# Kernel tuning notes

Measured on AMD Instinct MI355X. Metric: run time of the kernel, lower is better.

## Reference

```python
import jax, jax.numpy as jnp
import numpy as np

H = 1024
F = 4096  # base_ffn_dim = hidden * 4
WIDTHS = [256, 512]  # adapters; idx 2 -> width==hidden -> identity
EPS = 1e-5


def _xavier(key, fan_in, fan_out, gain):
    a = gain * np.sqrt(6.0 / (fan_in + fan_out))
    return jax.random.uniform(key, (fan_in, fan_out), jnp.float32, -a, a)


def _layernorm(x, g, b):
    mu = jnp.mean(x, axis=-1, keepdims=True)
    var = jnp.var(x, axis=-1, keepdims=True)
    return (x - mu) * jax.lax.rsqrt(var + EPS) * g + b


def setup_inputs() -> dict:
    key = jax.random.key(0)
    ks = jax.random.split(key, 12)
    g = 1.0 / np.sqrt(2.0)
    B, S = 4, 2048
    return {
        "x": jax.random.normal(ks[0], (B, S, H), jnp.float32),
        "width_multiplier": jax.random.uniform(ks[1], (B, S, 1), jnp.float32),
        "width_idx": jax.random.randint(ks[2], (B, S), 0, 3, jnp.int32),
        "ln_in_g": jnp.ones((H,), jnp.float32),
        "ln_in_b": jnp.zeros((H,), jnp.float32),
        "W1": _xavier(ks[3], H, F, g),
        "b1": jnp.zeros((F,), jnp.float32),
        "ln_h_g": jnp.ones((F,), jnp.float32),
        "ln_h_b": jnp.zeros((F,), jnp.float32),
        "W2": _xavier(ks[4], F, H, g),
        "b2": jnp.zeros((H,), jnp.float32),
        "a256_w1": _xavier(ks[5], H, 256, g),
        "a256_b1": jnp.zeros((256,), jnp.float32),
        "a256_w2": _xavier(ks[6], 256, H, g),
        "a256_b2": jnp.zeros((H,), jnp.float32),
        "a512_w1": _xavier(ks[7], H, 512, g),
        "a512_b1": jnp.zeros((512,), jnp.float32),
        "a512_w2": _xavier(ks[8], 512, H, g),
        "a512_b2": jnp.zeros((H,), jnp.float32),
    }


def reference(x, width_multiplier, width_idx,
              ln_in_g, ln_in_b, W1, b1, ln_h_g, ln_h_b, W2, b2,
              a256_w1, a256_b1, a256_w2, a256_b2,
              a512_w1, a512_b1, a512_w2, a512_b2):
    gelu = lambda t: jax.nn.gelu(t, approximate=False)  # torch nn.GELU exact
    x_norm = _layernorm(x, ln_in_g, ln_in_b)
    # base FFN path
    h = gelu(jnp.einsum("bsh,hf->bsf", x_norm, W1) + b1)
    h = _layernorm(h, ln_h_g, ln_h_b)
    base = jnp.einsum("bsf,fh->bsh", h, W2) + b2
    # width adapters (routed per token by width_idx)
    ad0 = jnp.einsum("bsw,wh->bsh", gelu(jnp.einsum("bsh,hw->bsw", x_norm, a256_w1) + a256_b1), a256_w2) + a256_b2
    ad1 = jnp.einsum("bsw,wh->bsh", gelu(jnp.einsum("bsh,hw->bsw", x_norm, a512_w1) + a512_b1), a512_w2) + a512_b2
    idx = width_idx[..., None]
    adaptive = jnp.where(idx == 0, ad0, jnp.where(idx == 1, ad1, x_norm))
    return base * width_multiplier + adaptive * (1.0 - width_multiplier)
```

## Files before the change

### kernel.cpp

```cpp
#include <hip/hip_runtime.h>
#include <cstdint>
#include <cstddef>

typedef unsigned short u16x8 __attribute__((ext_vector_type(8)));
typedef unsigned short u16x4 __attribute__((ext_vector_type(4)));
typedef __bf16 bf16x8 __attribute__((ext_vector_type(8)));
typedef float f32x4 __attribute__((ext_vector_type(4)));

__device__ __forceinline__ float b2f(unsigned short u) {
    union { unsigned int i; float f; } v;
    v.i = ((unsigned int)u) << 16;
    return v.f;
}

__device__ __forceinline__ unsigned short f2b(float f) {
    union { float f; unsigned int i; } v;
    v.f = f;
    unsigned int x = v.i;
    unsigned int lsb = (x >> 16) & 1u;
    x += 0x7FFFu + lsb;
    return (unsigned short)(x >> 16);
}

__device__ __forceinline__ float gelu_exact(float x) {
    return 0.5f * x * (1.0f + erff(x * 0.70710678118654752f));
}

__device__ __forceinline__ void ld_lds16(const unsigned short* g, unsigned short* l) {
    __builtin_amdgcn_global_load_lds(
        (const __attribute__((address_space(1))) void*)g,
        (__attribute__((address_space(3))) void*)l, 16, 0, 0);
}

__global__ void transpose_f32_bf16(const float* __restrict__ in,
                                   unsigned short* __restrict__ out, int R, int C,
                                   const float* __restrict__ scale) {
    __shared__ float tile[32][33];
    int x = blockIdx.x * 32 + threadIdx.x;
    int y0 = blockIdx.y * 32;
    for (int k = 0; k < 32; k += 8)
        tile[threadIdx.y + k][threadIdx.x] = in[(size_t)(y0 + threadIdx.y + k) * C + x];
    __syncthreads();
    int ox = y0 + threadIdx.x;
    int oy = blockIdx.x * 32;
    float sc = scale ? scale[ox] : 1.0f;
    for (int k = 0; k < 32; k += 8)
        out[(size_t)(oy + threadIdx.y + k) * R + ox] = f2b(tile[threadIdx.x][threadIdx.y + k] * sc);
}

__global__ void concat_bias(const float* __restrict__ b0, const float* __restrict__ b1,
                            float* __restrict__ out) {
    int t = threadIdx.x + blockIdx.x * blockDim.x;
    if (t < 256) out[t] = b0[t];
    else if (t < 768) out[t] = b1[t - 256];
}

__global__ void init_c01(const float* __restrict__ b2, float* __restrict__ c0b2,
                         float* __restrict__ c1) {
    int n = blockIdx.x * 256 + threadIdx.x;
    c0b2[n] = b2[n];
    c1[n] = 0.0f;
}

__global__ void prep_c01(const float* __restrict__ W2, const float* __restrict__ g,
                         const float* __restrict__ b, float* __restrict__ c0b2,
                         float* __restrict__ c1, int K, int N) {
    int n = blockIdx.x * 256 + threadIdx.x;
    int k0 = blockIdx.y * 256;
    float p0 = 0.f, p1 = 0.f;
    for (int k = k0; k < k0 + 256; ++k) {
        float w = W2[(size_t)k * N + n];
        p0 += b[k] * w;
        p1 += g[k] * w;
    }
    atomicAdd(&c0b2[n], p0);
    atomicAdd(&c1[n], p1);
}

__global__ __launch_bounds__(256) void rowstats4096(const unsigned short* __restrict__ h,
                                                    float* __restrict__ st) {
    const int row = blockIdx.x;
    const int t = threadIdx.x;
    const u16x8* p = (const u16x8*)(h + (size_t)row * 4096);
    float s = 0.f, s2 = 0.f;
#pragma unroll
    for (int i = 0; i < 2; ++i) {
        u16x8 v = p[t + (i << 8)];
#pragma unroll
        for (int r = 0; r < 8; ++r) { float f = b2f(v[r]); s += f; s2 += f * f; }
    }
#pragma unroll
    for (int o = 32; o > 0; o >>= 1) {
        s  += __shfl_down(s, o, 64);
        s2 += __shfl_down(s2, o, 64);
    }
    __shared__ float red[8];
    int lane = t & 63, w = t >> 6;
    if (lane == 0) { red[w] = s; red[4 + w] = s2; }
    __syncthreads();
    if (t == 0) {
        float ss = red[0] + red[1] + red[2] + red[3];
        float qq = red[4] + red[5] + red[6] + red[7];
        const float inv = 1.0f / 4096.0f;
        float mu = ss * inv;
        float var = qq * inv - mu * mu;
        float rs = rsqrtf(var + 1e-5f);
        st[2 * (size_t)row]     = rs;
        st[2 * (size_t)row + 1] = rs * mu;
    }
}

__global__ __launch_bounds__(256) void ln1024(const float* __restrict__ in,
                                              unsigned short* __restrict__ out,
                                              const float* __restrict__ g,
                                              const float* __restrict__ b) {
    const int row = blockIdx.x;
    const int t = threadIdx.x;
    f32x4 v = ((const f32x4*)(in + (size_t)row * 1024))[t];
    float s = v[0] + v[1] + v[2] + v[3];
    float s2 = v[0] * v[0] + v[1] * v[1] + v[2] * v[2] + v[3] * v[3];
#pragma unroll
    for (int o = 32; o > 0; o >>= 1) {
        s  += __shfl_down(s, o, 64);
        s2 += __shfl_down(s2, o, 64);
    }
    __shared__ float red[8];
    int lane = t & 63, w = t >> 6;
    if (lane == 0) { red[w] = s; red[4 + w] = s2; }
    __syncthreads();
    if (t == 0) {
        red[0] = red[0] + red[1] + red[2] + red[3];
        red[4] = red[4] + red[5] + red[6] + red[7];
    }
    __syncthreads();
    const float inv_n = 1.0f / 1024.0f;
    float mu = red[0] * inv_n;
    float var = red[4] * inv_n - mu * mu;
    float rs = rsqrtf(var + 1e-5f);
    f32x4 gv = ((const f32x4*)g)[t];
    f32x4 bv = ((const f32x4*)b)[t];
    u16x4 ov;
#pragma unroll
    for (int r = 0; r < 4; ++r) ov[r] = f2b((v[r] - mu) * rs * gv[r] + bv[r]);
    ((u16x4*)(out + (size_t)row * 1024))[t] = ov;
}

__global__ __launch_bounds__(512, 2) void gemm256_gelu(
    const unsigned short* __restrict__ A, int lda,
    const unsigned short* __restrict__ BT, int ldb,
    const float* __restrict__ bias, unsigned short* __restrict__ Cb,
    int M, int N, int K) {
    __shared__ __align__(16) unsigned short As[2][256 * 64];
    __shared__ __align__(16) unsigned short Bs[2][256 * 64];

    const int t = threadIdx.x;

    int id = blockIdx.y * gridDim.x + blockIdx.x;
    const int nwg = gridDim.x * gridDim.y;
    {
        const int cpx = nwg >> 3;
        id = (id & 7) * cpx + (id >> 3);
    }
    const int m0 = (id / gridDim.x) * 256;
    const int n0 = (id % gridDim.x) * 256;

    const int lane = t & 63;
    const int wid = t >> 6;
    const int wmr = (wid >> 2) << 7;
    const int wnr = (wid & 3) << 6;
    const int ml = lane & 15;
    const int q = lane >> 4;

    const int srow8 = lane >> 3;
    const int scol = (((lane & 7) ^ (srow8 & 7)) << 3);

    const int c0 = ((q ^ (ml & 7)) << 3);
    const int c1 = c0 ^ 32;

    f32x4 acc[8][4];
#pragma unroll
    for (int i = 0; i < 8; ++i)
#pragma unroll
        for (int j = 0; j < 4; ++j)
#pragma unroll
            for (int r = 0; r < 4; ++r) acc[i][j][r] = 0.0f;

    const int nk = K >> 6;

#define STAGE256(KT, BUF)                                                       \
    {                                                                           \
        const unsigned short* asrc =                                            \
            A + (size_t)(m0 + wid * 8 + srow8) * lda + (KT) * 64 + scol;        \
        const unsigned short* bsrc =                                            \
            BT + (size_t)(n0 + wid * 8 + srow8) * ldb + (KT) * 64 + scol;       \
        _Pragma("unroll")                                                       \
        for (int s = 0; s < 4; ++s) {                                           \
            ld_lds16(asrc + (size_t)s * 64 * lda, &As[BUF][(s * 64 + wid * 8) * 64]); \
            ld_lds16(bsrc + (size_t)s * 64 * ldb, &Bs[BUF][(s * 64 + wid * 8) * 64]); \
        }                                                                       \
    }

#define LDA256(QI)                                                              \
    _Pragma("unroll")                                                           \
    for (int i2 = 0; i2 < 4; ++i2) {                                            \
        int row = wmr + (QI) * 64 + i2 * 16 + ml;                               \
        afq[i2][0] = *(const bf16x8*)(&As[cur][(row << 6) + c0]);               \
        afq[i2][1] = *(const bf16x8*)(&As[cur][(row << 6) + c1]);               \
    }

#define LDB256(DST, QJ)                                                         \
    _Pragma("unroll")                                                           \
    for (int j2 = 0; j2 < 2; ++j2) {                                            \
        int row = wnr + (QJ) * 32 + j2 * 16 + ml;                               \
        DST[j2][0] = *(const bf16x8*)(&Bs[cur][(row << 6) + c0]);               \
        DST[j2][1] = *(const bf16x8*)(&Bs[cur][(row << 6) + c1]);               \
    }

#define MFMA16(I0, J0, BF)                                                      \
    __builtin_amdgcn_s_barrier();                                               \
    __builtin_amdgcn_s_setprio(1);                                              \
    _Pragma("unroll")                                                           \
    for (int i2 = 0; i2 < 4; ++i2)                                              \
        _Pragma("unroll")                                                       \
        for (int j2 = 0; j2 < 2; ++j2) {                                        \
            acc[(I0) + i2][(J0) + j2] = __builtin_amdgcn_mfma_f32_16x16x32_bf16( \
                afq[i2][0], BF[j2][0], acc[(I0) + i2][(J0) + j2], 0, 0, 0);     \
            acc[(I0) + i2][(J0) + j2] = __builtin_amdgcn_mfma_f32_16x16x32_bf16( \
                afq[i2][1], BF[j2][1], acc[(I0) + i2][(J0) + j2], 0, 0, 0);     \
        }                                                                       \
    __builtin_amdgcn_s_setprio(0);                                              \
    __builtin_amdgcn_s_barrier();

    STAGE256(0, 0);
    for (int kt = 0; kt < nk; ++kt) {
        const int cur = kt & 1;
        if (kt + 1 < nk) {
            STAGE256(kt + 1, cur ^ 1);
            asm volatile("s_waitcnt vmcnt(8)" ::: "memory");
        } else {
            asm volatile("s_waitcnt vmcnt(0)" ::: "memory");
        }
        __builtin_amdgcn_s_barrier();

        bf16x8 afq[4][2], b0f[2][2], b1f[2][2];
        LDA256(0);
        LDB256(b0f, 0);
        MFMA16(0, 0, b0f);
        LDB256(b1f, 1);
        MFMA16(0, 2, b1f);
        LDA256(1);
        MFMA16(4, 2, b1f);
        MFMA16(4, 0, b0f);
    }
#undef STAGE256
#undef LDA256
#undef LDB256
#undef MFMA16

#pragma unroll
    for (int i = 0; i < 8; ++i) {
#pragma unroll
        for (int j = 0; j < 4; ++j) {
            int col = n0 + wnr + j * 16 + ml;
            float bv = bias[col];
#pragma unroll
            for (int r = 0; r < 4; ++r) {
                int row = m0 + wmr + i * 16 + q * 4 + r;
                Cb[(size_t)row * N + col] = f2b(gelu_exact(acc[i][j][r] + bv));
            }
        }
    }
}

template <int EPI>
__global__ __launch_bounds__(256) void gemm_bt(
    const unsigned short* __restrict__ A, int lda,
    const unsigned short* __restrict__ BT, int ldb,
    const float* __restrict__ bias, unsigned short* __restrict__ Cb,
    float* __restrict__ Cf, int M, int N, int K,
    const int* __restrict__ idx, int match,
    const float* __restrict__ wm,
    const unsigned short* __restrict__ adaptive,
    const unsigned short* __restrict__ xn,
    const float* __restrict__ c1v,
    const float* __restrict__ rstat) {
    __shared__ __align__(16) unsigned short As[2][128 * 32];
    __shared__ __align__(16) unsigned short Bs[2][128 * 32];

    const int t = threadIdx.x;

    int id = blockIdx.y * gridDim.x + blockIdx.x;
    const int nwg = gridDim.x * gridDim.y;
    if ((nwg & 7) == 0) {
        const int cpx = nwg >> 3;
        id = (id & 7) * cpx + (id >> 3);
    }
    const int bx = id % gridDim.x;
    const int by = id / gridDim.x;
    const int m0 = by * 128;
    const int n0 = bx * 128;

    const int lane = t & 63;
    const int wid = t >> 6;

    const int srow = lane >> 2;
    const int sch  = (lane & 3) ^ (srow & 3);
    const int scol = sch << 3;

    const int wr = (wid >> 1) << 6;
    const int wc = (wid & 1) << 6;
    const int ml = lane & 15;
    const int q = lane >> 4;
    const int qsw = ((q ^ (ml & 3)) << 3);

    f32x4 acc[4][4];
#pragma unroll
    for (int i = 0; i < 4; ++i)
#pragma unroll
        for (int j = 0; j < 4; ++j)
#pragma unroll
            for (int r = 0; r < 4; ++r) acc[i][j][r] = 0.0f;

    const int nk = K >> 5;

#define STAGE(KT, BUF)                                                          \
    {                                                                           \
        _Pragma("unroll")                                                       \
        for (int hh = 0; hh < 2; ++hh) {                                        \
            int rbase = wid * 32 + hh * 16;                                     \
            int row = rbase + srow;                                             \
            ld_lds16(A  + (size_t)(m0 + row) * lda + (KT) * 32 + scol,          \
                     &As[BUF][rbase * 32]);                                     \
            ld_lds16(BT + (size_t)(n0 + row) * ldb + (KT) * 32 + scol,          \
                     &Bs[BUF][rbase * 32]);                                     \
        }                                                                       \
    }

    STAGE(0, 0);
    for (int kt = 0; kt < nk; ++kt) {
        const int cur = kt & 1;
        __syncthreads();
        if (kt + 1 < nk) STAGE(kt + 1, cur ^ 1);

        bf16x8 af[4], bf[4];
#pragma unroll
        for (int i = 0; i < 4; ++i)
            af[i] = *(const bf16x8*)(&As[cur][(wr + i * 16 + ml) * 32 + qsw]);
#pragma unroll
        for (int j = 0; j < 4; ++j)
            bf[j] = *(const bf16x8*)(&Bs[cur][(wc + j * 16 + ml) * 32 + qsw]);
#pragma unroll
        for (int i = 0; i < 4; ++i)
#pragma unroll
            for (int j = 0; j < 4; ++j)
                acc[i][j] = __builtin_amdgcn_mfma_f32_16x16x32_bf16(af[i], bf[j], acc[i][j], 0, 0, 0);
    }
#undef STAGE

#pragma unroll
    for (int i = 0; i < 4; ++i) {
        float rsv[4], rmv[4], wv[4];
        int idv[4];
        if (EPI == 1 || EPI == 2) {
#pragma unroll
            for (int r = 0; r < 4; ++r) {
                int row = m0 + wr + i * 16 + q * 4 + r;
                idv[r] = idx[row];
                if (EPI == 2) {
                    wv[r] = wm[row];
                    rsv[r] = rstat[2 * (size_t)row];
                    rmv[r] = rstat[2 * (size_t)row + 1];
                }
            }
        }
#pragma unroll
        for (int j = 0; j < 4; ++j) {
            int col = n0 + wc + j * 16 + ml;
            float bv = bias[col];
            float c1c = (EPI == 2) ? c1v[col] : 0.0f;
#pragma unroll
            for (int r = 0; r < 4; ++r) {
                int row = m0 + wr + i * 16 + q * 4 + r;
                size_t off = (size_t)row * N + col;
                if (EPI == 0) {
                    Cb[off] = f2b(gelu_exact(acc[i][j][r] + bv));
                } else if (EPI == 1) {
                    if (idv[r] == match) Cb[off] = f2b(acc[i][j][r] + bv);
                } else {
                    float bval = rsv[r] * acc[i][j][r] + bv - rmv[r] * c1c;
                    float a = b2f((idv[r] <= 1) ? adaptive[off] : xn[off]);
                    Cf[off] = bval * wv[r] + a * (1.0f - wv[r]);
                }
            }
        }
    }
}

extern "C" void kernel_launch(void* const* d_in, const int* in_sizes, int n_in,
                              void* d_out, int out_size, void* d_ws, size_t ws_size,
                              hipStream_t stream) {
    const float* x       = (const float*)d_in[0];
    const float* wm      = (const float*)d_in[1];
    const int*   widx    = (const int*)d_in[2];
    const float* ln_in_g = (const float*)d_in[3];
    const float* ln_in_b = (const float*)d_in[4];
    const float* W1      = (const float*)d_in[5];
    const float* b1      = (const float*)d_in[6];
    const float* ln_h_g  = (const float*)d_in[7];
    const float* ln_h_b  = (const float*)d_in[8];
    const float* W2      = (const float*)d_in[9];
    const float* b2      = (const float*)d_in[10];
    const float* a256_w1 = (const float*)d_in[11];
    const float* a256_b1 = (const float*)d_in[12];
    const float* a256_w2 = (const float*)d_in[13];
    const float* a256_b2 = (const float*)d_in[14];
    const float* a512_w1 = (const float*)d_in[15];
    const float* a512_b1 = (const float*)d_in[16];
    const float* a512_w2 = (const float*)d_in[17];
    const float* a512_b2 = (const float*)d_in[18];
    float* out = (float*)d_out;

    const int T = 8192, H = 1024, F = 4096;

    unsigned short* ws0   = (unsigned short*)d_ws;
    unsigned short* xn    = ws0;
    unsigned short* h     = xn    + (size_t)T * H;
    unsigned short* tt    = h     + (size_t)T * F;
    unsigned short* adp   = tt    + (size_t)T * 768;
    unsigned short* W1T   = adp   + (size_t)T * H;
    unsigned short* W2T   = W1T   + (size_t)H * F;
    unsigned short* awup  = W2T   + (size_t)F * H;
    unsigned short* aw2T0 = awup  + (size_t)768 * H;
    unsigned short* aw2T1 = aw2T0 + (size_t)H * 256;
    float*          ab1   = (float*)(aw2T1 + (size_t)H * 512);
    float*          stats = ab1 + 768;
    float*          c0b2  = stats + (size_t)T * 2;
    float*          c1    = c0b2 + H;

    dim3 tb(32, 8);
    init_c01<<<H / 256, 256, 0, stream>>>(b2, c0b2, c1);
    prep_c01<<<dim3(H / 256, F / 256), 256, 0, stream>>>(W2, ln_h_g, ln_h_b, c0b2, c1, F, H);

    transpose_f32_bf16<<<dim3(F / 32,   H / 32), tb, 0, stream>>>(W1, W1T, H, F, nullptr);
    transpose_f32_bf16<<<dim3(H / 32,   F / 32), tb, 0, stream>>>(W2, W2T, F, H, ln_h_g);
    transpose_f32_bf16<<<dim3(256 / 32, H / 32), tb, 0, stream>>>(a256_w1, awup, H, 256, nullptr);
    transpose_f32_bf16<<<dim3(512 / 32, H / 32), tb, 0, stream>>>(a512_w1, awup + (size_t)256 * H, H, 512, nullptr);
    transpose_f32_bf16<<<dim3(H / 32, 256 / 32), tb, 0, stream>>>(a256_w2, aw2T0, 256, H, nullptr);
    transpose_f32_bf16<<<dim3(H / 32, 512 / 32), tb, 0, stream>>>(a512_w2, aw2T1, 512, H, nullptr);
    concat_bias<<<3, 256, 0, stream>>>(a256_b1, a512_b1, ab1);

    ln1024<<<T, 256, 0, stream>>>(x, xn, ln_in_g, ln_in_b);

    gemm256_gelu<<<dim3(F / 256, T / 256), 512, 0, stream>>>(
        xn, H, W1T, H, b1, h, T, F, H);

    rowstats4096<<<T, 256, 0, stream>>>(h, stats);

    gemm_bt<0><<<dim3(768 / 128, T / 128), 256, 0, stream>>>(
        xn, H, awup, H, ab1, tt, nullptr, T, 768, H, nullptr, 0, nullptr, nullptr, nullptr, nullptr, nullptr);

    gemm_bt<1><<<dim3(H / 128, T / 128), 256, 0, stream>>>(
        tt, 768, aw2T0, 256, a256_b2, adp, nullptr, T, H, 256, widx, 0, nullptr, nullptr, nullptr, nullptr, nullptr);
    gemm_bt<1><<<dim3(H / 128, T / 128), 256, 0, stream>>>(
        tt + 256, 768, aw2T1, 512, a512_b2, adp, nullptr, T, H, 512, widx, 1, nullptr, nullptr, nullptr, nullptr, nullptr);

    gemm_bt<2><<<dim3(H / 128, T / 128), 256, 0, stream>>>(
        h, F, W2T, F, c0b2, nullptr, out, T, H, F, widx, 0, wm, adp, xn, c1, stats);
}
```

Before: 471.5 us.

## Interleave next-tile global-to-LDS prefetch across MFMA phases in GEMM1 kernel

```diff
diff --git a/kernel.cpp b/kernel.cpp
--- a/kernel.cpp
+++ b/kernel.cpp
@@ -166,6 +166,7 @@
 
     const int lane = t & 63;
     const int wid = t >> 6;
+    const int wid8 = wid << 3;
     const int wmr = (wid >> 2) << 7;
     const int wnr = (wid & 3) << 6;
     const int ml = lane & 15;
@@ -187,37 +188,38 @@
 
     const int nk = K >> 6;
 
-#define STAGE256(KT, BUF)                                                       \
+#define STAGE_A(KT, BUF, HALF)                                                  \
     {                                                                           \
-        const unsigned short* asrc =                                            \
-            A + (size_t)(m0 + wid * 8 + srow8) * lda + (KT) * 64 + scol;        \
-        const unsigned short* bsrc =                                            \
-            BT + (size_t)(n0 + wid * 8 + srow8) * ldb + (KT) * 64 + scol;       \
-        _Pragma("unroll")                                                       \
-        for (int s = 0; s < 4; ++s) {                                           \
-            ld_lds16(asrc + (size_t)s * 64 * lda, &As[BUF][(s * 64 + wid * 8) * 64]); \
-            ld_lds16(bsrc + (size_t)s * 64 * ldb, &Bs[BUF][(s * 64 + wid * 8) * 64]); \
-        }                                                                       \
-    }
-
-#define LDA256(QI)                                                              \
+        const unsigned short* src =                                             \
+            A + (size_t)(m0 + (HALF) * 128 + wid8 + srow8) * lda + (KT) * 64 + scol; \
+        ld_lds16(src,                    &As[BUF][((HALF) * 128 + wid8) * 64]); \
+        ld_lds16(src + (size_t)64 * lda, &As[BUF][((HALF) * 128 + 64 + wid8) * 64]); \
+    }
+#define STAGE_B(KT, BUF, HALF)                                                  \
+    {                                                                           \
+        const unsigned short* src =                                             \
+            BT + (size_t)(n0 + (HALF) * 128 + wid8 + srow8) * ldb + (KT) * 64 + scol; \
+        ld_lds16(src,                    &Bs[BUF][((HALF) * 128 + wid8) * 64]); \
+        ld_lds16(src + (size_t)64 * ldb, &Bs[BUF][((HALF) * 128 + 64 + wid8) * 64]); \
+    }
+
+#define LDA8(RH)                                                                \
     _Pragma("unroll")                                                           \
     for (int i2 = 0; i2 < 4; ++i2) {                                            \
-        int row = wmr + (QI) * 64 + i2 * 16 + ml;                               \
+        int row = wmr + (RH) * 64 + i2 * 16 + ml;                               \
         afq[i2][0] = *(const bf16x8*)(&As[cur][(row << 6) + c0]);               \
         afq[i2][1] = *(const bf16x8*)(&As[cur][(row << 6) + c1]);               \
     }
 
-#define LDB256(DST, QJ)                                                         \
+#define LDB4(DST, CH)                                                           \
     _Pragma("unroll")                                                           \
     for (int j2 = 0; j2 < 2; ++j2) {                                            \
-        int row = wnr + (QJ) * 32 + j2 * 16 + ml;                               \
+        int row = wnr + (CH) * 32 + j2 * 16 + ml;                               \
         DST[j2][0] = *(const bf16x8*)(&Bs[cur][(row << 6) + c0]);               \
         DST[j2][1] = *(const bf16x8*)(&Bs[cur][(row << 6) + c1]);               \
     }
 
 #define MFMA16(I0, J0, BF)                                                      \
-    __builtin_amdgcn_s_barrier();                                               \
     __builtin_amdgcn_s_setprio(1);                                              \
     _Pragma("unroll")                                                           \
     for (int i2 = 0; i2 < 4; ++i2)                                              \
@@ -228,33 +230,50 @@
             acc[(I0) + i2][(J0) + j2] = __builtin_amdgcn_mfma_f32_16x16x32_bf16( \
                 afq[i2][1], BF[j2][1], acc[(I0) + i2][(J0) + j2], 0, 0, 0);     \
         }                                                                       \
-    __builtin_amdgcn_s_setprio(0);                                              \
-    __builtin_amdgcn_s_barrier();
-
-    STAGE256(0, 0);
+    __builtin_amdgcn_s_setprio(0);
+
+    STAGE_A(0, 0, 0);
+    STAGE_B(0, 0, 0);
+    STAGE_B(0, 0, 1);
+    STAGE_A(0, 0, 1);
+
     for (int kt = 0; kt < nk; ++kt) {
         const int cur = kt & 1;
-        if (kt + 1 < nk) {
-            STAGE256(kt + 1, cur ^ 1);
-            asm volatile("s_waitcnt vmcnt(8)" ::: "memory");
-        } else {
-            asm volatile("s_waitcnt vmcnt(0)" ::: "memory");
-        }
-        __builtin_amdgcn_s_barrier();
-
+        const int nxt = cur ^ 1;
+        const bool pf = (kt + 1 < nk);
         bf16x8 afq[4][2], b0f[2][2], b1f[2][2];
-        LDA256(0);
-        LDB256(b0f, 0);
+
+        asm volatile("s_waitcnt vmcnt(0)" ::: "memory");
+        __builtin_amdgcn_s_barrier();
+
+        LDA8(0);
+        LDB4(b0f, 0);
+        if (pf) STAGE_A(kt + 1, nxt, 0);
+        __builtin_amdgcn_s_barrier();
         MFMA16(0, 0, b0f);
-        LDB256(b1f, 1);
+        __builtin_amdgcn_s_barrier();
+
+        LDB4(b1f, 1);
+        if (pf) STAGE_B(kt + 1, nxt, 0);
+        __builtin_amdgcn_s_barrier();
         MFMA16(0, 2, b1f);
-        LDA256(1);
+        __builtin_amdgcn_s_barrier();
+
+        LDA8(1);
+        if (pf) STAGE_B(kt + 1, nxt, 1);
+        __builtin_amdgcn_s_barrier();
         MFMA16(4, 2, b1f);
+        __builtin_amdgcn_s_barrier();
+
+        if (pf) STAGE_A(kt + 1, nxt, 1);
+        __builtin_amdgcn_s_barrier();
         MFMA16(4, 0, b0f);
-    }
-#undef STAGE256
-#undef LDA256
-#undef LDB256
+        __builtin_amdgcn_s_barrier();
+    }
+#undef STAGE_A
+#undef STAGE_B
+#undef LDA8
+#undef LDB4
 #undef MFMA16
 
 #pragma unroll
```

Measured after the change: 578.8 us. 22.8% more time.
